# Performance work log

Measured on AMD Instinct MI355X. Metric: run time of the kernel, lower is better.

Reference implementation:

```python
import jax, jax.numpy as jnp
import numpy as np

B, S, E, H, DK, DV, DF = 4, 2048, 512, 8, 64, 64, 2048
EPS = 1e-3  # keras LayerNormalization default epsilon


def setup_inputs() -> dict:
    key = jax.random.key(0)
    ks = jax.random.split(key, 24)
    def n(k, shape, scale=0.02):
        return jax.random.normal(k, shape, jnp.float32) * scale
    inp = {}
    inp["x"] = jax.random.normal(ks[0], (B, S, E), jnp.float32)
    inp["encoder_output"] = jax.random.normal(ks[1], (B, S, E), jnp.float32)
    # lookahead mask: 1 above the diagonal (masked), broadcast over batch/heads
    inp["lookahead_mask"] = jnp.triu(jnp.ones((S, S), jnp.int32), k=1)[None, None]
    # padding mask: 0 = keep (no padding in this synthetic batch)
    inp["padding_mask"] = jnp.zeros((B, 1, 1, S), jnp.int32)
    # self-attention params
    inp["sa_Wq"] = n(ks[2], (E, H * DK)); inp["sa_bq"] = jnp.zeros((H * DK,), jnp.float32)
    inp["sa_Wk"] = n(ks[3], (E, H * DK)); inp["sa_bk"] = jnp.zeros((H * DK,), jnp.float32)
    inp["sa_Wv"] = n(ks[4], (E, H * DV)); inp["sa_bv"] = jnp.zeros((H * DV,), jnp.float32)
    inp["sa_Wo"] = n(ks[5], (H * DV, E)); inp["sa_bo"] = jnp.zeros((E,), jnp.float32)
    # cross-attention params
    inp["ca_Wq"] = n(ks[6], (E, H * DK)); inp["ca_bq"] = jnp.zeros((H * DK,), jnp.float32)
    inp["ca_Wk"] = n(ks[7], (E, H * DK)); inp["ca_bk"] = jnp.zeros((H * DK,), jnp.float32)
    inp["ca_Wv"] = n(ks[8], (E, H * DV)); inp["ca_bv"] = jnp.zeros((H * DV,), jnp.float32)
    inp["ca_Wo"] = n(ks[9], (H * DV, E)); inp["ca_bo"] = jnp.zeros((E,), jnp.float32)
    # feed-forward params
    inp["ff_W1"] = n(ks[10], (E, DF)); inp["ff_b1"] = jnp.zeros((DF,), jnp.float32)
    inp["ff_W2"] = n(ks[11], (DF, E)); inp["ff_b2"] = jnp.zeros((E,), jnp.float32)
    # layernorm params (3 add&norm blocks)
    for i in (1, 2, 3):
        inp[f"ln{i}_g"] = jnp.ones((E,), jnp.float32)
        inp[f"ln{i}_b"] = jnp.zeros((E,), jnp.float32)
    return inp


def _mha(q_in, k_in, v_in, mask, Wq, bq, Wk, bk, Wv, bv, Wo, bo):
    Bq, Sq, _ = q_in.shape
    Sk = k_in.shape[1]
    q = (q_in @ Wq + bq).reshape(Bq, Sq, H, DK).transpose(0, 2, 1, 3)  # bhqd
    k = (k_in @ Wk + bk).reshape(Bq, Sk, H, DK).transpose(0, 2, 1, 3)  # bhkd
    v = (v_in @ Wv + bv).reshape(Bq, Sk, H, DV).transpose(0, 2, 1, 3)  # bhkd
    scores = jnp.einsum("bhqd,bhkd->bhqk", q, k) / jnp.sqrt(jnp.float32(DK))
    scores = scores - 1e9 * mask.astype(scores.dtype)  # additive mask (1 = masked)
    attn = jax.nn.softmax(scores, axis=-1)
    out = jnp.einsum("bhqk,bhkd->bhqd", attn, v)
    out = out.transpose(0, 2, 1, 3).reshape(Bq, Sq, H * DV)
    return out @ Wo + bo


def _add_norm(x, sub, g, b):
    y = x + sub
    m = jnp.mean(y, axis=-1, keepdims=True)
    v = jnp.var(y, axis=-1, keepdims=True)
    return (y - m) / jnp.sqrt(v + EPS) * g + b


def reference(x, encoder_output, lookahead_mask, padding_mask,
              sa_Wq, sa_bq, sa_Wk, sa_bk, sa_Wv, sa_bv, sa_Wo, sa_bo,
              ca_Wq, ca_bq, ca_Wk, ca_bk, ca_Wv, ca_bv, ca_Wo, ca_bo,
              ff_W1, ff_b1, ff_W2, ff_b2,
              ln1_g, ln1_b, ln2_g, ln2_b, ln3_g, ln3_b):
    # dropout is identity at inference (training=False)
    a1 = _mha(x, x, x, lookahead_mask,
              sa_Wq, sa_bq, sa_Wk, sa_bk, sa_Wv, sa_bv, sa_Wo, sa_bo)
    x1 = _add_norm(x, a1, ln1_g, ln1_b)
    a2 = _mha(x1, encoder_output, encoder_output, padding_mask,
              ca_Wq, ca_bq, ca_Wk, ca_bk, ca_Wv, ca_bv, ca_Wo, ca_bo)
    x2 = _add_norm(x1, a2, ln2_g, ln2_b)
    ff = jax.nn.relu(x2 @ ff_W1 + ff_b1) @ ff_W2 + ff_b2
    return _add_norm(x2, ff, ln3_g, ln3_b)
```

## Files before the change

### kernel.cpp

```cpp
#include <hip/hip_runtime.h>

#define Bx  4
#define Sx  2048
#define Ex  512
#define Hx  8
#define Tt  (Bx * Sx)

typedef short          short8 __attribute__((ext_vector_type(8)));
typedef float          f32x4  __attribute__((ext_vector_type(4)));
typedef unsigned short u16;

__device__ __forceinline__ u16 f2bf(float f) {
    unsigned int u = __float_as_uint(f);
    u += 0x7fffu + ((u >> 16) & 1u);
    return (u16)(u >> 16);
}
__device__ __forceinline__ float bf2f(u16 h) {
    return __uint_as_float(((unsigned int)h) << 16);
}

__global__ __launch_bounds__(256) void f32_to_bf16(const float* __restrict__ in,
                                                   u16* __restrict__ out)
{
    int i = (blockIdx.x * 256 + threadIdx.x) << 2;
    float4 v = *(const float4*)(in + i);
    ushort4 o;
    o.x = f2bf(v.x); o.y = f2bf(v.y); o.z = f2bf(v.z); o.w = f2bf(v.w);
    *(ushort4*)(out + i) = o;
}

__global__ __launch_bounds__(256) void transpose_bf16(const float* __restrict__ W,
                                                      u16* __restrict__ Wt,
                                                      int K, int N)
{
    __shared__ u16 tile[32][33];
    const int n0 = blockIdx.x * 32, k0 = blockIdx.y * 32;
    const int tx = threadIdx.x & 31, ty = threadIdx.x >> 5;
#pragma unroll
    for (int i = 0; i < 32; i += 8)
        tile[ty + i][tx] = f2bf(W[(size_t)(k0 + ty + i) * N + n0 + tx]);
    __syncthreads();
#pragma unroll
    for (int i = 0; i < 32; i += 8)
        Wt[(size_t)(n0 + ty + i) * K + k0 + tx] = tile[tx][ty + i];
}

template<int OUT_BF16, int RELU>
__global__ __launch_bounds__(256) void gemm_mfma(const u16* __restrict__ A,
                                                 const u16* __restrict__ Bt,
                                                 const float* __restrict__ bias,
                                                 void* __restrict__ Cout,
                                                 int M, int N, int K)
{
    __shared__ u16 As[128 * 40];
    __shared__ u16 Bs[128 * 40];

    const int tid  = threadIdx.x;
    const int w    = tid >> 6;
    const int lane = tid & 63;
    const int c    = lane & 15;
    const int quad = lane >> 4;
    const int wr   = w >> 1, wc = w & 1;
    const int m0   = blockIdx.y * 128;
    const int n0   = blockIdx.x * 128;

    const int row0 = tid >> 2;
    const int kc   = (tid & 3) << 3;

    const u16* Ap = A  + (size_t)(m0 + row0) * K + kc;
    const u16* Bp = Bt + (size_t)(n0 + row0) * K + kc;
    const size_t rstep = (size_t)64 * K;

    f32x4 acc[4][4];
#pragma unroll
    for (int i = 0; i < 4; i++)
#pragma unroll
        for (int j = 0; j < 4; j++) { acc[i][j][0]=0.f; acc[i][j][1]=0.f; acc[i][j][2]=0.f; acc[i][j][3]=0.f; }

    short8 ra0 = *(const short8*)(Ap);
    short8 ra1 = *(const short8*)(Ap + rstep);
    short8 rb0 = *(const short8*)(Bp);
    short8 rb1 = *(const short8*)(Bp + rstep);

    for (int k0 = 0; k0 < K; k0 += 32) {
        __syncthreads();
        *(short8*)&As[row0 * 40 + kc]        = ra0;
        *(short8*)&As[(row0 + 64) * 40 + kc] = ra1;
        *(short8*)&Bs[row0 * 40 + kc]        = rb0;
        *(short8*)&Bs[(row0 + 64) * 40 + kc] = rb1;
        __syncthreads();

        if (k0 + 32 < K) {
            ra0 = *(const short8*)(Ap + k0 + 32);
            ra1 = *(const short8*)(Ap + rstep + k0 + 32);
            rb0 = *(const short8*)(Bp + k0 + 32);
            rb1 = *(const short8*)(Bp + rstep + k0 + 32);
        }

        short8 af[4], bf[4];
#pragma unroll
        for (int i = 0; i < 4; i++)
            af[i] = *(const short8*)&As[(wr * 64 + i * 16 + c) * 40 + quad * 8];
#pragma unroll
        for (int j = 0; j < 4; j++)
            bf[j] = *(const short8*)&Bs[(wc * 64 + j * 16 + c) * 40 + quad * 8];
#pragma unroll
        for (int i = 0; i < 4; i++)
#pragma unroll
            for (int j = 0; j < 4; j++)
                acc[i][j] = __builtin_amdgcn_mfma_f32_16x16x32_bf16(af[i], bf[j], acc[i][j], 0, 0, 0);
    }

    float bv[4];
#pragma unroll
    for (int j = 0; j < 4; j++) bv[j] = bias[n0 + wc * 64 + j * 16 + c];

#pragma unroll
    for (int i = 0; i < 4; i++) {
#pragma unroll
        for (int j = 0; j < 4; j++) {
            int colg = n0 + wc * 64 + j * 16 + c;
#pragma unroll
            for (int r = 0; r < 4; r++) {
                int rowg = m0 + wr * 64 + i * 16 + quad * 4 + r;
                float v = acc[i][j][r] + bv[j];
                if (RELU) v = fmaxf(v, 0.f);
                if (OUT_BF16) ((u16*)Cout)[(size_t)rowg * N + colg] = f2bf(v);
                else          ((float*)Cout)[(size_t)rowg * N + colg] = v;
            }
        }
    }
}

template<bool CAUSAL>
__global__ __launch_bounds__(256) void attn_mfma(const u16* __restrict__ Q,
                                                 const u16* __restrict__ K,
                                                 const u16* __restrict__ V,
                                                 u16* __restrict__ O)
{
    __shared__ u16 Klds[32 * 72];
    __shared__ u16 Vtlds[64 * 40];
    __shared__ u16 Plds[4][16 * 40];

    const int tid  = threadIdx.x;
    const int w    = tid >> 6;
    const int lane = tid & 63;
    const int c    = lane & 15;
    const int quad = lane >> 4;
    const int q0   = blockIdx.x * 64;
    const int bh   = blockIdx.y;
    const int b    = bh >> 3;
    const int h    = bh & 7;
    const int bS   = b * Sx;
    const int hoff = h * 64;

    const int kkey = tid >> 3;
    const int kc8  = (tid & 7) << 3;
    const int vdim = tid & 63;
    const int vkg  = tid >> 6;

    const u16* qp = Q + (size_t)(bS + q0 + w * 16 + c) * Ex + hoff;
    short8 qa[2];
    qa[0] = *(const short8*)(qp + quad * 8);
    qa[1] = *(const short8*)(qp + 32 + quad * 8);

    f32x4 of[4];
#pragma unroll
    for (int f = 0; f < 4; f++) { of[f][0]=0.f; of[f][1]=0.f; of[f][2]=0.f; of[f][3]=0.f; }
    float lpart[4] = {0.f, 0.f, 0.f, 0.f};

    const int kend = CAUSAL ? (q0 + 64) : Sx;
    for (int kt = 0; kt < kend; kt += 32) {
        __syncthreads();
        *(short8*)&Klds[kkey * 72 + kc8] =
            *(const short8*)(K + (size_t)(bS + kt + kkey) * Ex + hoff + kc8);
        {
            const u16* gv = V + (size_t)(bS + kt + vkg * 8) * Ex + hoff + vdim;
            union { short8 v; u16 u[8]; } vb;
#pragma unroll
            for (int j = 0; j < 8; j++) vb.u[j] = gv[(size_t)j * Ex];
            *(short8*)&Vtlds[vdim * 40 + vkg * 8] = vb.v;
        }
        __syncthreads();

        f32x4 s[2];
#pragma unroll
        for (int kf = 0; kf < 2; kf++) {
            short8 kb0 = *(const short8*)&Klds[(kf * 16 + c) * 72 + quad * 8];
            short8 kb1 = *(const short8*)&Klds[(kf * 16 + c) * 72 + 32 + quad * 8];
            f32x4 z; z[0]=0.f; z[1]=0.f; z[2]=0.f; z[3]=0.f;
            z = __builtin_amdgcn_mfma_f32_16x16x32_bf16(qa[0], kb0, z, 0, 0, 0);
            z = __builtin_amdgcn_mfma_f32_16x16x32_bf16(qa[1], kb1, z, 0, 0, 0);
            s[kf] = z;
        }

#pragma unroll
        for (int kf = 0; kf < 2; kf++) {
            int key_abs = kt + kf * 16 + c;
#pragma unroll
            for (int r = 0; r < 4; r++) {
                float p;
                if (CAUSAL && key_abs > (q0 + w * 16 + quad * 4 + r)) p = 0.f;
                else p = __expf(s[kf][r] * 0.125f);
                u16 pb = f2bf(p);
                lpart[r] += bf2f(pb);
                Plds[w][(quad * 4 + r) * 40 + kf * 16 + c] = pb;
            }
        }
        __threadfence_block();

        short8 pa = *(const short8*)&Plds[w][c * 40 + quad * 8];
#pragma unroll
        for (int f = 0; f < 4; f++) {
            int dim = f * 16 + c;
            short8 vb = *(const short8*)&Vtlds[dim * 40 + quad * 8];
            of[f] = __builtin_amdgcn_mfma_f32_16x16x32_bf16(pa, vb, of[f], 0, 0, 0);
        }
    }

#pragma unroll
    for (int r = 0; r < 4; r++) {
        float v = lpart[r];
        v += __shfl_xor(v, 1, 64);
        v += __shfl_xor(v, 2, 64);
        v += __shfl_xor(v, 4, 64);
        v += __shfl_xor(v, 8, 64);
        lpart[r] = 1.f / v;
    }

    u16* Ob = O + (size_t)(bS + q0 + w * 16) * Ex + hoff;
#pragma unroll
    for (int f = 0; f < 4; f++) {
#pragma unroll
        for (int r = 0; r < 4; r++) {
            Ob[(size_t)(quad * 4 + r) * Ex + f * 16 + c] = f2bf(of[f][r] * lpart[r]);
        }
    }
}

__global__ __launch_bounds__(256) void ln_add(const float* __restrict__ x,
                                              const float* __restrict__ s,
                                              const float* __restrict__ g,
                                              const float* __restrict__ bta,
                                              float* __restrict__ out,
                                              u16* __restrict__ out_bf)
{
    __shared__ float red[8];
    const int    row  = blockIdx.x;
    const int    t    = threadIdx.x;
    const size_t base = (size_t)row * Ex;

    float2 xv = *(const float2*)(x + base + (t << 1));
    float2 sv = *(const float2*)(s + base + (t << 1));
    float  y0 = xv.x + sv.x;
    float  y1 = xv.y + sv.y;

    float sum = y0 + y1;
    float sq  = y0 * y0 + y1 * y1;
#pragma unroll
    for (int o = 32; o > 0; o >>= 1) {
        sum += __shfl_down(sum, o, 64);
        sq  += __shfl_down(sq,  o, 64);
    }
    const int wid = t >> 6, lane = t & 63;
    if (lane == 0) { red[wid] = sum; red[4 + wid] = sq; }
    __syncthreads();
    if (t == 0) {
        red[0] = red[0] + red[1] + red[2] + red[3];
        red[4] = red[4] + red[5] + red[6] + red[7];
    }
    __syncthreads();

    const float mean = red[0] * (1.f / 512.f);
    const float var  = red[4] * (1.f / 512.f) - mean * mean;
    const float rstd = rsqrtf(var + 1e-3f);

    float2 gv = *(const float2*)(g   + (t << 1));
    float2 bv = *(const float2*)(bta + (t << 1));
    float  o0 = (y0 - mean) * rstd * gv.x + bv.x;
    float  o1 = (y1 - mean) * rstd * gv.y + bv.y;
    *(float2*)(out + base + (t << 1)) = make_float2(o0, o1);
    if (out_bf) {
        ushort2 ob; ob.x = f2bf(o0); ob.y = f2bf(o1);
        *(ushort2*)(out_bf + base + (t << 1)) = ob;
    }
}

extern "C" void kernel_launch(void* const* d_in, const int* in_sizes, int n_in,
                              void* d_out, int out_size, void* d_ws, size_t ws_size,
                              hipStream_t stream)
{
    const float* x     = (const float*)d_in[0];
    const float* enc   = (const float*)d_in[1];
    const float* sa_Wq = (const float*)d_in[4],  *sa_bq = (const float*)d_in[5];
    const float* sa_Wk = (const float*)d_in[6],  *sa_bk = (const float*)d_in[7];
    const float* sa_Wv = (const float*)d_in[8],  *sa_bv = (const float*)d_in[9];
    const float* sa_Wo = (const float*)d_in[10], *sa_bo = (const float*)d_in[11];
    const float* ca_Wq = (const float*)d_in[12], *ca_bq = (const float*)d_in[13];
    const float* ca_Wk = (const float*)d_in[14], *ca_bk = (const float*)d_in[15];
    const float* ca_Wv = (const float*)d_in[16], *ca_bv = (const float*)d_in[17];
    const float* ca_Wo = (const float*)d_in[18], *ca_bo = (const float*)d_in[19];
    const float* ff_W1 = (const float*)d_in[20], *ff_b1 = (const float*)d_in[21];
    const float* ff_W2 = (const float*)d_in[22], *ff_b2 = (const float*)d_in[23];
    const float* ln1_g = (const float*)d_in[24], *ln1_b = (const float*)d_in[25];
    const float* ln2_g = (const float*)d_in[26], *ln2_b = (const float*)d_in[27];
    const float* ln3_g = (const float*)d_in[28], *ln3_b = (const float*)d_in[29];

    char* ws = (char*)d_ws;
    const size_t MB = 1024 * 1024;
    u16*   bw   = (u16*)(ws);
    u16*   xb   = (u16*)(ws + 8  * MB);
    u16*   encb = (u16*)(ws + 16 * MB);
    u16*   qb   = (u16*)(ws + 24 * MB);
    u16*   kb   = (u16*)(ws + 32 * MB);
    u16*   vb   = (u16*)(ws + 40 * MB);
    u16*   ob   = (u16*)(ws + 48 * MB);
    float* proj = (float*)(ws + 56 * MB);
    float* x1f  = (float*)(ws + 72 * MB);
    u16*   x1b  = (u16*)(ws + 88 * MB);
    float* x2f  = (float*)(ws + 8  * MB);
    u16*   x2b  = (u16*)(ws + 48 * MB);
    u16*   ff1b = (u16*)(ws + 56 * MB);
    float* ff2f = (float*)(ws + 24 * MB);

    u16* wsaq = bw;                 u16* wsak = bw + 262144;
    u16* wsav = bw + 524288;        u16* wsao = bw + 786432;
    u16* wcaq = bw + 1048576;       u16* wcak = bw + 1310720;
    u16* wcav = bw + 1572864;       u16* wcao = bw + 1835008;
    u16* wff1 = bw + 2097152;       u16* wff2 = bw + 3145728;

    f32_to_bf16<<<dim3(Tt * Ex / 1024), dim3(256), 0, stream>>>(x,   xb);
    f32_to_bf16<<<dim3(Tt * Ex / 1024), dim3(256), 0, stream>>>(enc, encb);
    auto TR = [&](const float* W, u16* Wt, int K, int N) {
        transpose_bf16<<<dim3(N / 32, K / 32), dim3(256), 0, stream>>>(W, Wt, K, N);
    };
    TR(sa_Wq, wsaq, 512, 512);  TR(sa_Wk, wsak, 512, 512);
    TR(sa_Wv, wsav, 512, 512);  TR(sa_Wo, wsao, 512, 512);
    TR(ca_Wq, wcaq, 512, 512);  TR(ca_Wk, wcak, 512, 512);
    TR(ca_Wv, wcav, 512, 512);  TR(ca_Wo, wcao, 512, 512);
    TR(ff_W1, wff1, 512, 2048); TR(ff_W2, wff2, 2048, 512);

    auto GEMM_BF = [&](const u16* A, const u16* Wt, const float* bi, u16* C,
                       int M, int N, int K, bool relu) {
        dim3 grid(N / 128, M / 128);
        if (relu) gemm_mfma<1, 1><<<grid, dim3(256), 0, stream>>>(A, Wt, bi, C, M, N, K);
        else      gemm_mfma<1, 0><<<grid, dim3(256), 0, stream>>>(A, Wt, bi, C, M, N, K);
    };
    auto GEMM_F32 = [&](const u16* A, const u16* Wt, const float* bi, float* C,
                        int M, int N, int K) {
        dim3 grid(N / 128, M / 128);
        gemm_mfma<0, 0><<<grid, dim3(256), 0, stream>>>(A, Wt, bi, C, M, N, K);
    };
    const dim3 agrid(Sx / 64, Bx * Hx);

    GEMM_BF(xb, wsaq, sa_bq, qb, Tt, 512, 512, false);
    GEMM_BF(xb, wsak, sa_bk, kb, Tt, 512, 512, false);
    GEMM_BF(xb, wsav, sa_bv, vb, Tt, 512, 512, false);
    attn_mfma<true><<<agrid, dim3(256), 0, stream>>>(qb, kb, vb, ob);
    GEMM_F32(ob, wsao, sa_bo, proj, Tt, 512, 512);
    ln_add<<<dim3(Tt), dim3(256), 0, stream>>>(x, proj, ln1_g, ln1_b, x1f, x1b);

    GEMM_BF(x1b,  wcaq, ca_bq, qb, Tt, 512, 512, false);
    GEMM_BF(encb, wcak, ca_bk, kb, Tt, 512, 512, false);
    GEMM_BF(encb, wcav, ca_bv, vb, Tt, 512, 512, false);
    attn_mfma<false><<<agrid, dim3(256), 0, stream>>>(qb, kb, vb, ob);
    GEMM_F32(ob, wcao, ca_bo, proj, Tt, 512, 512);
    ln_add<<<dim3(Tt), dim3(256), 0, stream>>>(x1f, proj, ln2_g, ln2_b, x2f, x2b);

    GEMM_BF(x2b, wff1, ff_b1, ff1b, Tt, 2048, 512, true);
    GEMM_F32(ff1b, wff2, ff_b2, ff2f, Tt, 512, 2048);
    ln_add<<<dim3(Tt), dim3(256), 0, stream>>>(x2f, ff2f, ln3_g, ln3_b,
                                               (float*)d_out, (u16*)nullptr);
}
```

Measured before the change: 538.1 us.

## Retile GEMM to 128x64 two-wave blocks and widen attention to 128 queries

The GEMM now uses 128-thread blocks computing 128x64 tiles (each wave 64x64) and takes a leading-dimension argument. Q/K/V projections write into interleaved buffers so attention reads strided rows. The attention kernel now gives each wave 32 query rows, sharing K/V LDS tiles across twice the queries, packs P as bf16 pairs, and skips fully masked causal subtiles. The aim is less K/V reload traffic and better MFMA reuse. The costs are an extra block-wide barrier per key tile, fewer waves per GEMM block, and half as many attention blocks.

```diff
diff --git a/kernel.cpp b/kernel.cpp
--- a/kernel.cpp
+++ b/kernel.cpp
@@ -8,6 +8,7 @@
 
 typedef short          short8 __attribute__((ext_vector_type(8)));
 typedef float          f32x4  __attribute__((ext_vector_type(4)));
+typedef unsigned int   u32x4  __attribute__((ext_vector_type(4)));
 typedef unsigned short u16;
 
 __device__ __forceinline__ u16 f2bf(float f) {
@@ -46,30 +47,29 @@
 }
 
 template<int OUT_BF16, int RELU>
-__global__ __launch_bounds__(256) void gemm_mfma(const u16* __restrict__ A,
+__global__ __launch_bounds__(128) void gemm_mfma(const u16* __restrict__ A,
                                                  const u16* __restrict__ Bt,
                                                  const float* __restrict__ bias,
                                                  void* __restrict__ Cout,
-                                                 int M, int N, int K)
+                                                 int M, int N, int K, int ldc)
 {
     __shared__ u16 As[128 * 40];
-    __shared__ u16 Bs[128 * 40];
+    __shared__ u16 Bs[64 * 40];
 
     const int tid  = threadIdx.x;
     const int w    = tid >> 6;
     const int lane = tid & 63;
     const int c    = lane & 15;
     const int quad = lane >> 4;
-    const int wr   = w >> 1, wc = w & 1;
     const int m0   = blockIdx.y * 128;
-    const int n0   = blockIdx.x * 128;
-
-    const int row0 = tid >> 2;
-    const int kc   = (tid & 3) << 3;
-
-    const u16* Ap = A  + (size_t)(m0 + row0) * K + kc;
-    const u16* Bp = Bt + (size_t)(n0 + row0) * K + kc;
-    const size_t rstep = (size_t)64 * K;
+    const int n0   = blockIdx.x * 64;
+
+    const int rA = tid >> 2;
+    const int kc = (tid & 3) << 3;
+
+    const u16* Ap = A  + (size_t)(m0 + rA) * K + kc;
+    const u16* Bp = Bt + (size_t)(n0 + rA) * K + kc;
+    const size_t a32 = (size_t)32 * K;
 
     f32x4 acc[4][4];
 #pragma unroll
@@ -77,33 +77,34 @@
 #pragma unroll
         for (int j = 0; j < 4; j++) { acc[i][j][0]=0.f; acc[i][j][1]=0.f; acc[i][j][2]=0.f; acc[i][j][3]=0.f; }
 
-    short8 ra0 = *(const short8*)(Ap);
-    short8 ra1 = *(const short8*)(Ap + rstep);
-    short8 rb0 = *(const short8*)(Bp);
-    short8 rb1 = *(const short8*)(Bp + rstep);
+    short8 ra[4], rb[2];
+#pragma unroll
+    for (int i = 0; i < 4; i++) ra[i] = *(const short8*)(Ap + i * a32);
+#pragma unroll
+    for (int i = 0; i < 2; i++) rb[i] = *(const short8*)(Bp + i * a32);
 
     for (int k0 = 0; k0 < K; k0 += 32) {
         __syncthreads();
-        *(short8*)&As[row0 * 40 + kc]        = ra0;
-        *(short8*)&As[(row0 + 64) * 40 + kc] = ra1;
-        *(short8*)&Bs[row0 * 40 + kc]        = rb0;
-        *(short8*)&Bs[(row0 + 64) * 40 + kc] = rb1;
+#pragma unroll
+        for (int i = 0; i < 4; i++) *(short8*)&As[(rA + i * 32) * 40 + kc] = ra[i];
+#pragma unroll
+        for (int i = 0; i < 2; i++) *(short8*)&Bs[(rA + i * 32) * 40 + kc] = rb[i];
         __syncthreads();
 
         if (k0 + 32 < K) {
-            ra0 = *(const short8*)(Ap + k0 + 32);
-            ra1 = *(const short8*)(Ap + rstep + k0 + 32);
-            rb0 = *(const short8*)(Bp + k0 + 32);
-            rb1 = *(const short8*)(Bp + rstep + k0 + 32);
+#pragma unroll
+            for (int i = 0; i < 4; i++) ra[i] = *(const short8*)(Ap + i * a32 + k0 + 32);
+#pragma unroll
+            for (int i = 0; i < 2; i++) rb[i] = *(const short8*)(Bp + i * a32 + k0 + 32);
         }
 
         short8 af[4], bf[4];
 #pragma unroll
         for (int i = 0; i < 4; i++)
-            af[i] = *(const short8*)&As[(wr * 64 + i * 16 + c) * 40 + quad * 8];
+            af[i] = *(const short8*)&As[(w * 64 + i * 16 + c) * 40 + quad * 8];
 #pragma unroll
         for (int j = 0; j < 4; j++)
-            bf[j] = *(const short8*)&Bs[(wc * 64 + j * 16 + c) * 40 + quad * 8];
+            bf[j] = *(const short8*)&Bs[(j * 16 + c) * 40 + quad * 8];
 #pragma unroll
         for (int i = 0; i < 4; i++)
 #pragma unroll
@@ -113,20 +114,20 @@
 
     float bv[4];
 #pragma unroll
-    for (int j = 0; j < 4; j++) bv[j] = bias[n0 + wc * 64 + j * 16 + c];
+    for (int j = 0; j < 4; j++) bv[j] = bias[n0 + j * 16 + c];
 
 #pragma unroll
     for (int i = 0; i < 4; i++) {
 #pragma unroll
         for (int j = 0; j < 4; j++) {
-            int colg = n0 + wc * 64 + j * 16 + c;
+            int colg = n0 + j * 16 + c;
 #pragma unroll
             for (int r = 0; r < 4; r++) {
-                int rowg = m0 + wr * 64 + i * 16 + quad * 4 + r;
+                int rowg = m0 + w * 64 + i * 16 + quad * 4 + r;
                 float v = acc[i][j][r] + bv[j];
                 if (RELU) v = fmaxf(v, 0.f);
-                if (OUT_BF16) ((u16*)Cout)[(size_t)rowg * N + colg] = f2bf(v);
-                else          ((float*)Cout)[(size_t)rowg * N + colg] = v;
+                if (OUT_BF16) ((u16*)Cout)[(size_t)rowg * ldc + colg] = f2bf(v);
+                else          ((float*)Cout)[(size_t)rowg * ldc + colg] = v;
             }
         }
     }
@@ -136,105 +137,141 @@
 __global__ __launch_bounds__(256) void attn_mfma(const u16* __restrict__ Q,
                                                  const u16* __restrict__ K,
                                                  const u16* __restrict__ V,
-                                                 u16* __restrict__ O)
-{
-    __shared__ u16 Klds[32 * 72];
-    __shared__ u16 Vtlds[64 * 40];
-    __shared__ u16 Plds[4][16 * 40];
+                                                 u16* __restrict__ O,
+                                                 int ldq, int ldk, int ldv)
+{
+    __shared__ u16          Klds[32 * 72];
+    __shared__ u16          Vtlds[64 * 40];
+    __shared__ unsigned int Plds[4][32 * 20];
 
     const int tid  = threadIdx.x;
     const int w    = tid >> 6;
     const int lane = tid & 63;
     const int c    = lane & 15;
     const int quad = lane >> 4;
-    const int q0   = blockIdx.x * 64;
+    const int q0   = blockIdx.x * 128;
     const int bh   = blockIdx.y;
     const int b    = bh >> 3;
     const int h    = bh & 7;
     const int bS   = b * Sx;
     const int hoff = h * 64;
+    const int qw   = q0 + w * 32;
 
     const int kkey = tid >> 3;
     const int kc8  = (tid & 7) << 3;
     const int vdim = tid & 63;
-    const int vkg  = tid >> 6;
-
-    const u16* qp = Q + (size_t)(bS + q0 + w * 16 + c) * Ex + hoff;
-    short8 qa[2];
-    qa[0] = *(const short8*)(qp + quad * 8);
-    qa[1] = *(const short8*)(qp + 32 + quad * 8);
-
-    f32x4 of[4];
-#pragma unroll
-    for (int f = 0; f < 4; f++) { of[f][0]=0.f; of[f][1]=0.f; of[f][2]=0.f; of[f][3]=0.f; }
-    float lpart[4] = {0.f, 0.f, 0.f, 0.f};
-
-    const int kend = CAUSAL ? (q0 + 64) : Sx;
+    const int vp   = (tid >> 6) << 3;
+    const int kb2  = vp >> 1;
+
+    short8 qa[2][2];
+#pragma unroll
+    for (int rf = 0; rf < 2; rf++) {
+        const u16* qp = Q + (size_t)(bS + qw + rf * 16 + c) * ldq + hoff;
+        qa[rf][0] = *(const short8*)(qp + quad * 8);
+        qa[rf][1] = *(const short8*)(qp + 32 + quad * 8);
+    }
+
+    f32x4 of[2][4];
+#pragma unroll
+    for (int rf = 0; rf < 2; rf++)
+#pragma unroll
+        for (int f = 0; f < 4; f++) { of[rf][f][0]=0.f; of[rf][f][1]=0.f; of[rf][f][2]=0.f; of[rf][f][3]=0.f; }
+    float lpart[2][4] = {{0.f,0.f,0.f,0.f},{0.f,0.f,0.f,0.f}};
+
+    const int kend = CAUSAL ? (q0 + 128) : Sx;
     for (int kt = 0; kt < kend; kt += 32) {
         __syncthreads();
         *(short8*)&Klds[kkey * 72 + kc8] =
-            *(const short8*)(K + (size_t)(bS + kt + kkey) * Ex + hoff + kc8);
+            *(const short8*)(K + (size_t)(bS + kt + kkey) * ldk + hoff + kc8);
         {
-            const u16* gv = V + (size_t)(bS + kt + vkg * 8) * Ex + hoff + vdim;
+            const u16* gv = V + (size_t)(bS + kt) * ldv + hoff + vdim;
             union { short8 v; u16 u[8]; } vb;
 #pragma unroll
-            for (int j = 0; j < 8; j++) vb.u[j] = gv[(size_t)j * Ex];
-            *(short8*)&Vtlds[vdim * 40 + vkg * 8] = vb.v;
+            for (int j = 0; j < 8; j++) {
+                int key = kb2 + (j >> 1) + ((j & 1) << 4);
+                vb.u[j] = gv[(size_t)key * ldv];
+            }
+            *(short8*)&Vtlds[vdim * 40 + vp] = vb.v;
         }
         __syncthreads();
 
-        f32x4 s[2];
-#pragma unroll
-        for (int kf = 0; kf < 2; kf++) {
-            short8 kb0 = *(const short8*)&Klds[(kf * 16 + c) * 72 + quad * 8];
-            short8 kb1 = *(const short8*)&Klds[(kf * 16 + c) * 72 + 32 + quad * 8];
-            f32x4 z; z[0]=0.f; z[1]=0.f; z[2]=0.f; z[3]=0.f;
-            z = __builtin_amdgcn_mfma_f32_16x16x32_bf16(qa[0], kb0, z, 0, 0, 0);
-            z = __builtin_amdgcn_mfma_f32_16x16x32_bf16(qa[1], kb1, z, 0, 0, 0);
-            s[kf] = z;
-        }
-
-#pragma unroll
-        for (int kf = 0; kf < 2; kf++) {
-            int key_abs = kt + kf * 16 + c;
-#pragma unroll
-            for (int r = 0; r < 4; r++) {
-                float p;
-                if (CAUSAL && key_abs > (q0 + w * 16 + quad * 4 + r)) p = 0.f;
-                else p = __expf(s[kf][r] * 0.125f);
-                u16 pb = f2bf(p);
-                lpart[r] += bf2f(pb);
-                Plds[w][(quad * 4 + r) * 40 + kf * 16 + c] = pb;
+        const bool live1 = !CAUSAL || (kt <= qw + 31);
+        const bool live0 = !CAUSAL || (kt <= qw + 15);
+
+        if (live1) {
+            short8 kb[2][2];
+#pragma unroll
+            for (int kf = 0; kf < 2; kf++) {
+                kb[kf][0] = *(const short8*)&Klds[(kf * 16 + c) * 72 + quad * 8];
+                kb[kf][1] = *(const short8*)&Klds[(kf * 16 + c) * 72 + 32 + quad * 8];
             }
-        }
-        __threadfence_block();
-
-        short8 pa = *(const short8*)&Plds[w][c * 40 + quad * 8];
-#pragma unroll
-        for (int f = 0; f < 4; f++) {
-            int dim = f * 16 + c;
-            short8 vb = *(const short8*)&Vtlds[dim * 40 + quad * 8];
-            of[f] = __builtin_amdgcn_mfma_f32_16x16x32_bf16(pa, vb, of[f], 0, 0, 0);
-        }
-    }
-
-#pragma unroll
-    for (int r = 0; r < 4; r++) {
-        float v = lpart[r];
-        v += __shfl_xor(v, 1, 64);
-        v += __shfl_xor(v, 2, 64);
-        v += __shfl_xor(v, 4, 64);
-        v += __shfl_xor(v, 8, 64);
-        lpart[r] = 1.f / v;
-    }
-
-    u16* Ob = O + (size_t)(bS + q0 + w * 16) * Ex + hoff;
-#pragma unroll
-    for (int f = 0; f < 4; f++) {
+
+#pragma unroll
+            for (int rf = 0; rf < 2; rf++) {
+                if (rf == 0 && !live0) continue;
+                f32x4 s[2];
+#pragma unroll
+                for (int kf = 0; kf < 2; kf++) {
+                    f32x4 z; z[0]=0.f; z[1]=0.f; z[2]=0.f; z[3]=0.f;
+                    z = __builtin_amdgcn_mfma_f32_16x16x32_bf16(qa[rf][0], kb[kf][0], z, 0, 0, 0);
+                    z = __builtin_amdgcn_mfma_f32_16x16x32_bf16(qa[rf][1], kb[kf][1], z, 0, 0, 0);
+                    s[kf] = z;
+                }
+#pragma unroll
+                for (int r = 0; r < 4; r++) {
+                    int qg = qw + rf * 16 + quad * 4 + r;
+                    float p0, p1;
+                    if (CAUSAL && (kt + c) > qg) p0 = 0.f;
+                    else p0 = __expf(s[0][r] * 0.125f);
+                    if (CAUSAL && (kt + 16 + c) > qg) p1 = 0.f;
+                    else p1 = __expf(s[1][r] * 0.125f);
+                    u16 b0 = f2bf(p0), b1 = f2bf(p1);
+                    lpart[rf][r] += bf2f(b0) + bf2f(b1);
+                    Plds[w][(rf * 16 + quad * 4 + r) * 20 + c] =
+                        (unsigned int)b0 | ((unsigned int)b1 << 16);
+                }
+            }
+        }
+        __syncthreads();
+
+        if (live1) {
+            short8 vb[4];
+#pragma unroll
+            for (int f = 0; f < 4; f++)
+                vb[f] = *(const short8*)&Vtlds[(f * 16 + c) * 40 + quad * 8];
+#pragma unroll
+            for (int rf = 0; rf < 2; rf++) {
+                if (rf == 0 && !live0) continue;
+                union { u32x4 u; short8 s; } pu;
+                pu.u = *(const u32x4*)&Plds[w][(rf * 16 + c) * 20 + quad * 4];
+                short8 pa = pu.s;
+#pragma unroll
+                for (int f = 0; f < 4; f++)
+                    of[rf][f] = __builtin_amdgcn_mfma_f32_16x16x32_bf16(pa, vb[f], of[rf][f], 0, 0, 0);
+            }
+        }
+    }
+
+#pragma unroll
+    for (int rf = 0; rf < 2; rf++)
 #pragma unroll
         for (int r = 0; r < 4; r++) {
-            Ob[(size_t)(quad * 4 + r) * Ex + f * 16 + c] = f2bf(of[f][r] * lpart[r]);
-        }
+            float v = lpart[rf][r];
+            v += __shfl_xor(v, 1, 64);
+            v += __shfl_xor(v, 2, 64);
+            v += __shfl_xor(v, 4, 64);
+            v += __shfl_xor(v, 8, 64);
+            lpart[rf][r] = 1.f / v;
+        }
+
+#pragma unroll
+    for (int rf = 0; rf < 2; rf++) {
+        u16* Ob = O + (size_t)(bS + qw + rf * 16) * Ex + hoff;
+#pragma unroll
+        for (int f = 0; f < 4; f++)
+#pragma unroll
+            for (int r = 0; r < 4; r++)
+                Ob[(size_t)(quad * 4 + r) * Ex + f * 16 + c] = f2bf(of[rf][f][r] * lpart[rf][r]);
     }
 }
 
@@ -311,17 +348,16 @@
     u16*   bw   = (u16*)(ws);
     u16*   xb   = (u16*)(ws + 8  * MB);
     u16*   encb = (u16*)(ws + 16 * MB);
+    u16*   qkvB = (u16*)(ws + 24 * MB);
     u16*   qb   = (u16*)(ws + 24 * MB);
-    u16*   kb   = (u16*)(ws + 32 * MB);
-    u16*   vb   = (u16*)(ws + 40 * MB);
+    u16*   kvB  = (u16*)(ws + 32 * MB);
+    u16*   ff1b = (u16*)(ws + 24 * MB);
     u16*   ob   = (u16*)(ws + 48 * MB);
-    float* proj = (float*)(ws + 56 * MB);
+    float* projF= (float*)(ws + 56 * MB);
     float* x1f  = (float*)(ws + 72 * MB);
     u16*   x1b  = (u16*)(ws + 88 * MB);
+    u16*   x2b  = (u16*)(ws + 88 * MB);
     float* x2f  = (float*)(ws + 8  * MB);
-    u16*   x2b  = (u16*)(ws + 48 * MB);
-    u16*   ff1b = (u16*)(ws + 56 * MB);
-    float* ff2f = (float*)(ws + 24 * MB);
 
     u16* wsaq = bw;                 u16* wsak = bw + 262144;
     u16* wsav = bw + 524288;        u16* wsao = bw + 786432;
@@ -340,35 +376,34 @@
     TR(ca_Wv, wcav, 512, 512);  TR(ca_Wo, wcao, 512, 512);
     TR(ff_W1, wff1, 512, 2048); TR(ff_W2, wff2, 2048, 512);
 
-    auto GEMM_BF = [&](const u16* A, const u16* Wt, const float* bi, u16* C,
-                       int M, int N, int K, bool relu) {
-        dim3 grid(N / 128, M / 128);
-        if (relu) gemm_mfma<1, 1><<<grid, dim3(256), 0, stream>>>(A, Wt, bi, C, M, N, K);
-        else      gemm_mfma<1, 0><<<grid, dim3(256), 0, stream>>>(A, Wt, bi, C, M, N, K);
+    auto GEMM = [&](const u16* A, const u16* Wt, const float* bi, void* C,
+                    int N, int K, int ldc, int out_bf, int relu) {
+        dim3 grid(N / 64, Tt / 128);
+        if (out_bf) {
+            if (relu) gemm_mfma<1,1><<<grid, dim3(128), 0, stream>>>(A, Wt, bi, C, Tt, N, K, ldc);
+            else      gemm_mfma<1,0><<<grid, dim3(128), 0, stream>>>(A, Wt, bi, C, Tt, N, K, ldc);
+        } else        gemm_mfma<0,0><<<grid, dim3(128), 0, stream>>>(A, Wt, bi, C, Tt, N, K, ldc);
     };
-    auto GEMM_F32 = [&](const u16* A, const u16* Wt, const float* bi, float* C,
-                        int M, int N, int K) {
-        dim3 grid(N / 128, M / 128);
-        gemm_mfma<0, 0><<<grid, dim3(256), 0, stream>>>(A, Wt, bi, C, M, N, K);
-    };
-    const dim3 agrid(Sx / 64, Bx * Hx);
-
-    GEMM_BF(xb, wsaq, sa_bq, qb, Tt, 512, 512, false);
-    GEMM_BF(xb, wsak, sa_bk, kb, Tt, 512, 512, false);
-    GEMM_BF(xb, wsav, sa_bv, vb, Tt, 512, 512, false);
-    attn_mfma<true><<<agrid, dim3(256), 0, stream>>>(qb, kb, vb, ob);
-    GEMM_F32(ob, wsao, sa_bo, proj, Tt, 512, 512);
-    ln_add<<<dim3(Tt), dim3(256), 0, stream>>>(x, proj, ln1_g, ln1_b, x1f, x1b);
-
-    GEMM_BF(x1b,  wcaq, ca_bq, qb, Tt, 512, 512, false);
-    GEMM_BF(encb, wcak, ca_bk, kb, Tt, 512, 512, false);
-    GEMM_BF(encb, wcav, ca_bv, vb, Tt, 512, 512, false);
-    attn_mfma<false><<<agrid, dim3(256), 0, stream>>>(qb, kb, vb, ob);
-    GEMM_F32(ob, wcao, ca_bo, proj, Tt, 512, 512);
-    ln_add<<<dim3(Tt), dim3(256), 0, stream>>>(x1f, proj, ln2_g, ln2_b, x2f, x2b);
-
-    GEMM_BF(x2b, wff1, ff_b1, ff1b, Tt, 2048, 512, true);
-    GEMM_F32(ff1b, wff2, ff_b2, ff2f, Tt, 512, 2048);
-    ln_add<<<dim3(Tt), dim3(256), 0, stream>>>(x2f, ff2f, ln3_g, ln3_b,
+    const dim3 agrid(Sx / 128, Bx * Hx);
+
+    GEMM(xb, wsaq, sa_bq, qkvB,        512, 512, 1536, 1, 0);
+    GEMM(xb, wsak, sa_bk, qkvB + 512,  512, 512, 1536, 1, 0);
+    GEMM(xb, wsav, sa_bv, qkvB + 1024, 512, 512, 1536, 1, 0);
+    attn_mfma<true><<<agrid, dim3(256), 0, stream>>>(qkvB, qkvB + 512, qkvB + 1024,
+                                                     ob, 1536, 1536, 1536);
+    GEMM(ob, wsao, sa_bo, projF, 512, 512, 512, 0, 0);
+    ln_add<<<dim3(Tt), dim3(256), 0, stream>>>(x, projF, ln1_g, ln1_b, x1f, x1b);
+
+    GEMM(x1b,  wcaq, ca_bq, qb,        512, 512, 512,  1, 0);
+    GEMM(encb, wcak, ca_bk, kvB,       512, 512, 1024, 1, 0);
+    GEMM(encb, wcav, ca_bv, kvB + 512, 512, 512, 1024, 1, 0);
+    attn_mfma<false><<<agrid, dim3(256), 0, stream>>>(qb, kvB, kvB + 512,
+                                                      ob, 512, 1024, 1024);
+    GEMM(ob, wcao, ca_bo, projF, 512, 512, 512, 0, 0);
+    ln_add<<<dim3(Tt), dim3(256), 0, stream>>>(x1f, projF, ln2_g, ln2_b, x2f, x2b);
+
+    GEMM(x2b, wff1, ff_b1, ff1b, 2048, 512, 2048, 1, 1);
+    GEMM(ff1b, wff2, ff_b2, projF, 512, 2048, 512, 0, 0);
+    ln_add<<<dim3(Tt), dim3(256), 0, stream>>>(x2f, projF, ln3_g, ln3_b,
                                                (float*)d_out, (u16*)nullptr);
 }
```

Result: slower. 583.1 us (+8.4%).

## Widen attention key tiles to 64, skip masked causal blocks, batch prep launches

Applied to the files above, without the earlier changes.

The attention kernel now processes 64 keys per iteration instead of 32, with larger K and V LDS tiles and a permuted V-transpose layout, so each P fragment packs two score blocks into 32-bit LDS words. It skips QK and PV MFMAs for 16-key blocks that lie entirely above the causal diagonal. Q/K/V projections write into interleaved strided buffers, and the input conversion and eight weight transposes are merged into fewer launches. The intent is to cut loop and synchronisation overhead per key and avoid wasted work on masked blocks. In exchange, LDS use per block is higher and the wave-local fence is replaced by a full __syncthreads.

```diff
diff --git a/kernel.cpp b/kernel.cpp
--- a/kernel.cpp
+++ b/kernel.cpp
@@ -8,6 +8,7 @@
 
 typedef short          short8 __attribute__((ext_vector_type(8)));
 typedef float          f32x4  __attribute__((ext_vector_type(4)));
+typedef unsigned int   u32x4  __attribute__((ext_vector_type(4)));
 typedef unsigned short u16;
 
 __device__ __forceinline__ u16 f2bf(float f) {
@@ -19,9 +20,13 @@
     return __uint_as_float(((unsigned int)h) << 16);
 }
 
-__global__ __launch_bounds__(256) void f32_to_bf16(const float* __restrict__ in,
-                                                   u16* __restrict__ out)
-{
+__global__ __launch_bounds__(256) void f32_to_bf16_2(const float* __restrict__ a,
+                                                     const float* __restrict__ b,
+                                                     u16* __restrict__ oa,
+                                                     u16* __restrict__ ob)
+{
+    const float* in  = blockIdx.y ? b : a;
+    u16*         out = blockIdx.y ? ob : oa;
     int i = (blockIdx.x * 256 + threadIdx.x) << 2;
     float4 v = *(const float4*)(in + i);
     ushort4 o;
@@ -45,12 +50,29 @@
         Wt[(size_t)(n0 + ty + i) * K + k0 + tx] = tile[tx][ty + i];
 }
 
+struct WPtrs { const float* w[8]; };
+__global__ __launch_bounds__(256) void transpose8_bf16(WPtrs ws, u16* __restrict__ base)
+{
+    __shared__ u16 tile[32][33];
+    const float* W  = ws.w[blockIdx.z];
+    u16*         Wt = base + (size_t)blockIdx.z * 262144;
+    const int n0 = blockIdx.x * 32, k0 = blockIdx.y * 32;
+    const int tx = threadIdx.x & 31, ty = threadIdx.x >> 5;
+#pragma unroll
+    for (int i = 0; i < 32; i += 8)
+        tile[ty + i][tx] = f2bf(W[(size_t)(k0 + ty + i) * 512 + n0 + tx]);
+    __syncthreads();
+#pragma unroll
+    for (int i = 0; i < 32; i += 8)
+        Wt[(size_t)(n0 + ty + i) * 512 + k0 + tx] = tile[tx][ty + i];
+}
+
 template<int OUT_BF16, int RELU>
 __global__ __launch_bounds__(256) void gemm_mfma(const u16* __restrict__ A,
                                                  const u16* __restrict__ Bt,
                                                  const float* __restrict__ bias,
                                                  void* __restrict__ Cout,
-                                                 int M, int N, int K)
+                                                 int M, int N, int K, int ldc)
 {
     __shared__ u16 As[128 * 40];
     __shared__ u16 Bs[128 * 40];
@@ -125,8 +147,8 @@
                 int rowg = m0 + wr * 64 + i * 16 + quad * 4 + r;
                 float v = acc[i][j][r] + bv[j];
                 if (RELU) v = fmaxf(v, 0.f);
-                if (OUT_BF16) ((u16*)Cout)[(size_t)rowg * N + colg] = f2bf(v);
-                else          ((float*)Cout)[(size_t)rowg * N + colg] = v;
+                if (OUT_BF16) ((u16*)Cout)[(size_t)rowg * ldc + colg] = f2bf(v);
+                else          ((float*)Cout)[(size_t)rowg * ldc + colg] = v;
             }
         }
     }
@@ -136,11 +158,12 @@
 __global__ __launch_bounds__(256) void attn_mfma(const u16* __restrict__ Q,
                                                  const u16* __restrict__ K,
                                                  const u16* __restrict__ V,
-                                                 u16* __restrict__ O)
-{
-    __shared__ u16 Klds[32 * 72];
-    __shared__ u16 Vtlds[64 * 40];
-    __shared__ u16 Plds[4][16 * 40];
+                                                 u16* __restrict__ O,
+                                                 int ldq, int ldk, int ldv)
+{
+    __shared__ u16          Klds[64 * 72];
+    __shared__ u16          Vtlds[64 * 72];
+    __shared__ unsigned int Plds[4][16 * 36];
 
     const int tid  = threadIdx.x;
     const int w    = tid >> 6;
@@ -153,16 +176,17 @@
     const int h    = bh & 7;
     const int bS   = b * Sx;
     const int hoff = h * 64;
-
-    const int kkey = tid >> 3;
-    const int kc8  = (tid & 7) << 3;
+    const int qw   = q0 + w * 16;
+
     const int vdim = tid & 63;
-    const int vkg  = tid >> 6;
-
-    const u16* qp = Q + (size_t)(bS + q0 + w * 16 + c) * Ex + hoff;
+    const int vp   = (tid >> 6) << 4;
+
     short8 qa[2];
-    qa[0] = *(const short8*)(qp + quad * 8);
-    qa[1] = *(const short8*)(qp + 32 + quad * 8);
+    {
+        const u16* qp = Q + (size_t)(bS + qw + c) * ldq + hoff;
+        qa[0] = *(const short8*)(qp + quad * 8);
+        qa[1] = *(const short8*)(qp + 32 + quad * 8);
+    }
 
     f32x4 of[4];
 #pragma unroll
@@ -170,51 +194,88 @@
     float lpart[4] = {0.f, 0.f, 0.f, 0.f};
 
     const int kend = CAUSAL ? (q0 + 64) : Sx;
-    for (int kt = 0; kt < kend; kt += 32) {
+    for (int kt = 0; kt < kend; kt += 64) {
         __syncthreads();
-        *(short8*)&Klds[kkey * 72 + kc8] =
-            *(const short8*)(K + (size_t)(bS + kt + kkey) * Ex + hoff + kc8);
+#pragma unroll
+        for (int i = 0; i < 2; i++) {
+            int chunk = tid + (i << 8);
+            int row   = chunk >> 3;
+            int c8    = (chunk & 7) << 3;
+            *(short8*)&Klds[row * 72 + c8] =
+                *(const short8*)(K + (size_t)(bS + kt + row) * ldk + hoff + c8);
+        }
         {
-            const u16* gv = V + (size_t)(bS + kt + vkg * 8) * Ex + hoff + vdim;
-            union { short8 v; u16 u[8]; } vb;
-#pragma unroll
-            for (int j = 0; j < 8; j++) vb.u[j] = gv[(size_t)j * Ex];
-            *(short8*)&Vtlds[vdim * 40 + vkg * 8] = vb.v;
+            const u16* gv = V + (size_t)(bS + kt) * ldv + hoff + vdim;
+            union { short8 v; u16 u[8]; } v0, v1;
+#pragma unroll
+            for (int j = 0; j < 8; j++) {
+                int pos = vp + j;
+                int g = pos >> 5, pp = pos & 31;
+                v0.u[j] = gv[(size_t)((g << 5) + (pp >> 1) + ((pp & 1) << 4)) * ldv];
+            }
+#pragma unroll
+            for (int j = 0; j < 8; j++) {
+                int pos = vp + 8 + j;
+                int g = pos >> 5, pp = pos & 31;
+                v1.u[j] = gv[(size_t)((g << 5) + (pp >> 1) + ((pp & 1) << 4)) * ldv];
+            }
+            *(short8*)&Vtlds[vdim * 72 + vp]     = v0.v;
+            *(short8*)&Vtlds[vdim * 72 + vp + 8] = v1.v;
         }
         __syncthreads();
 
-        f32x4 s[2];
-#pragma unroll
-        for (int kf = 0; kf < 2; kf++) {
-            short8 kb0 = *(const short8*)&Klds[(kf * 16 + c) * 72 + quad * 8];
-            short8 kb1 = *(const short8*)&Klds[(kf * 16 + c) * 72 + 32 + quad * 8];
-            f32x4 z; z[0]=0.f; z[1]=0.f; z[2]=0.f; z[3]=0.f;
-            z = __builtin_amdgcn_mfma_f32_16x16x32_bf16(qa[0], kb0, z, 0, 0, 0);
-            z = __builtin_amdgcn_mfma_f32_16x16x32_bf16(qa[1], kb1, z, 0, 0, 0);
-            s[kf] = z;
-        }
-
-#pragma unroll
-        for (int kf = 0; kf < 2; kf++) {
-            int key_abs = kt + kf * 16 + c;
-#pragma unroll
-            for (int r = 0; r < 4; r++) {
-                float p;
-                if (CAUSAL && key_abs > (q0 + w * 16 + quad * 4 + r)) p = 0.f;
-                else p = __expf(s[kf][r] * 0.125f);
-                u16 pb = f2bf(p);
-                lpart[r] += bf2f(pb);
-                Plds[w][(quad * 4 + r) * 40 + kf * 16 + c] = pb;
-            }
-        }
-        __threadfence_block();
-
-        short8 pa = *(const short8*)&Plds[w][c * 40 + quad * 8];
+        int fmax = 4;
+        if (CAUSAL) {
+            int d = ((qw + 15 - kt) >> 4) + 1;
+            fmax = d < 4 ? d : 4;
+        }
+
+        f32x4 s[4];
 #pragma unroll
         for (int f = 0; f < 4; f++) {
-            int dim = f * 16 + c;
-            short8 vb = *(const short8*)&Vtlds[dim * 40 + quad * 8];
-            of[f] = __builtin_amdgcn_mfma_f32_16x16x32_bf16(pa, vb, of[f], 0, 0, 0);
+            if (f < fmax) {
+                short8 kb0 = *(const short8*)&Klds[(f * 16 + c) * 72 + quad * 8];
+                short8 kb1 = *(const short8*)&Klds[(f * 16 + c) * 72 + 32 + quad * 8];
+                f32x4 z; z[0]=0.f; z[1]=0.f; z[2]=0.f; z[3]=0.f;
+                z = __builtin_amdgcn_mfma_f32_16x16x32_bf16(qa[0], kb0, z, 0, 0, 0);
+                z = __builtin_amdgcn_mfma_f32_16x16x32_bf16(qa[1], kb1, z, 0, 0, 0);
+                s[f] = z;
+            }
+        }
+
+#pragma unroll
+        for (int fp = 0; fp < 2; fp++) {
+            if (fp * 2 < fmax) {
+                int f0 = fp * 2, f1 = fp * 2 + 1;
+#pragma unroll
+                for (int r = 0; r < 4; r++) {
+                    int qg = qw + quad * 4 + r;
+                    float p0 = 0.f, p1 = 0.f;
+                    if (!(CAUSAL && (kt + f0 * 16 + c) > qg))
+                        p0 = __expf(s[f0][r] * 0.125f);
+                    if (f1 < fmax && !(CAUSAL && (kt + f1 * 16 + c) > qg))
+                        p1 = __expf(s[f1][r] * 0.125f);
+                    u16 b0 = f2bf(p0), b1 = f2bf(p1);
+                    lpart[r] += bf2f(b0) + bf2f(b1);
+                    Plds[w][(quad * 4 + r) * 36 + fp * 18 + c] =
+                        (unsigned int)b0 | ((unsigned int)b1 << 16);
+                }
+            }
+        }
+        __syncthreads();
+
+#pragma unroll
+        for (int g = 0; g < 2; g++) {
+            if (g * 2 < fmax) {
+                union { u32x4 u; short8 s; } pu;
+                pu.u = *(const u32x4*)&Plds[w][c * 36 + g * 18 + quad * 4];
+                short8 pa = pu.s;
+#pragma unroll
+                for (int f2 = 0; f2 < 4; f2++) {
+                    short8 vbf = *(const short8*)&Vtlds[(f2 * 16 + c) * 72 + (g << 5) + quad * 8];
+                    of[f2] = __builtin_amdgcn_mfma_f32_16x16x32_bf16(pa, vbf, of[f2], 0, 0, 0);
+                }
+            }
         }
     }
 
@@ -228,14 +289,12 @@
         lpart[r] = 1.f / v;
     }
 
-    u16* Ob = O + (size_t)(bS + q0 + w * 16) * Ex + hoff;
-#pragma unroll
-    for (int f = 0; f < 4; f++) {
-#pragma unroll
-        for (int r = 0; r < 4; r++) {
+    u16* Ob = O + (size_t)(bS + qw) * Ex + hoff;
+#pragma unroll
+    for (int f = 0; f < 4; f++)
+#pragma unroll
+        for (int r = 0; r < 4; r++)
             Ob[(size_t)(quad * 4 + r) * Ex + f * 16 + c] = f2bf(of[f][r] * lpart[r]);
-        }
-    }
 }
 
 __global__ __launch_bounds__(256) void ln_add(const float* __restrict__ x,
@@ -311,17 +370,16 @@
     u16*   bw   = (u16*)(ws);
     u16*   xb   = (u16*)(ws + 8  * MB);
     u16*   encb = (u16*)(ws + 16 * MB);
+    u16*   qkvB = (u16*)(ws + 24 * MB);
     u16*   qb   = (u16*)(ws + 24 * MB);
-    u16*   kb   = (u16*)(ws + 32 * MB);
-    u16*   vb   = (u16*)(ws + 40 * MB);
+    u16*   kvB  = (u16*)(ws + 32 * MB);
+    u16*   ff1b = (u16*)(ws + 24 * MB);
     u16*   ob   = (u16*)(ws + 48 * MB);
-    float* proj = (float*)(ws + 56 * MB);
+    float* projF= (float*)(ws + 56 * MB);
     float* x1f  = (float*)(ws + 72 * MB);
     u16*   x1b  = (u16*)(ws + 88 * MB);
+    u16*   x2b  = (u16*)(ws + 88 * MB);
     float* x2f  = (float*)(ws + 8  * MB);
-    u16*   x2b  = (u16*)(ws + 48 * MB);
-    u16*   ff1b = (u16*)(ws + 56 * MB);
-    float* ff2f = (float*)(ws + 24 * MB);
 
     u16* wsaq = bw;                 u16* wsak = bw + 262144;
     u16* wsav = bw + 524288;        u16* wsao = bw + 786432;
@@ -329,46 +387,41 @@
     u16* wcav = bw + 1572864;       u16* wcao = bw + 1835008;
     u16* wff1 = bw + 2097152;       u16* wff2 = bw + 3145728;
 
-    f32_to_bf16<<<dim3(Tt * Ex / 1024), dim3(256), 0, stream>>>(x,   xb);
-    f32_to_bf16<<<dim3(Tt * Ex / 1024), dim3(256), 0, stream>>>(enc, encb);
-    auto TR = [&](const float* W, u16* Wt, int K, int N) {
-        transpose_bf16<<<dim3(N / 32, K / 32), dim3(256), 0, stream>>>(W, Wt, K, N);
-    };
-    TR(sa_Wq, wsaq, 512, 512);  TR(sa_Wk, wsak, 512, 512);
-    TR(sa_Wv, wsav, 512, 512);  TR(sa_Wo, wsao, 512, 512);
-    TR(ca_Wq, wcaq, 512, 512);  TR(ca_Wk, wcak, 512, 512);
-    TR(ca_Wv, wcav, 512, 512);  TR(ca_Wo, wcao, 512, 512);
-    TR(ff_W1, wff1, 512, 2048); TR(ff_W2, wff2, 2048, 512);
-
-    auto GEMM_BF = [&](const u16* A, const u16* Wt, const float* bi, u16* C,
-                       int M, int N, int K, bool relu) {
-        dim3 grid(N / 128, M / 128);
-        if (relu) gemm_mfma<1, 1><<<grid, dim3(256), 0, stream>>>(A, Wt, bi, C, M, N, K);
-        else      gemm_mfma<1, 0><<<grid, dim3(256), 0, stream>>>(A, Wt, bi, C, M, N, K);
-    };
-    auto GEMM_F32 = [&](const u16* A, const u16* Wt, const float* bi, float* C,
-                        int M, int N, int K) {
-        dim3 grid(N / 128, M / 128);
-        gemm_mfma<0, 0><<<grid, dim3(256), 0, stream>>>(A, Wt, bi, C, M, N, K);
+    f32_to_bf16_2<<<dim3(Tt * Ex / 1024, 2), dim3(256), 0, stream>>>(x, enc, xb, encb);
+    WPtrs wp; wp.w[0]=sa_Wq; wp.w[1]=sa_Wk; wp.w[2]=sa_Wv; wp.w[3]=sa_Wo;
+    wp.w[4]=ca_Wq; wp.w[5]=ca_Wk; wp.w[6]=ca_Wv; wp.w[7]=ca_Wo;
+    transpose8_bf16<<<dim3(16, 16, 8), dim3(256), 0, stream>>>(wp, bw);
+    transpose_bf16<<<dim3(64, 16), dim3(256), 0, stream>>>(ff_W1, wff1, 512, 2048);
+    transpose_bf16<<<dim3(16, 64), dim3(256), 0, stream>>>(ff_W2, wff2, 2048, 512);
+
+    auto GEMM = [&](const u16* A, const u16* Wt, const float* bi, void* C,
+                    int N, int K, int ldc, int out_bf, int relu) {
+        dim3 grid(N / 128, Tt / 128);
+        if (out_bf) {
+            if (relu) gemm_mfma<1,1><<<grid, dim3(256), 0, stream>>>(A, Wt, bi, C, Tt, N, K, ldc);
+            else      gemm_mfma<1,0><<<grid, dim3(256), 0, stream>>>(A, Wt, bi, C, Tt, N, K, ldc);
+        } else        gemm_mfma<0,0><<<grid, dim3(256), 0, stream>>>(A, Wt, bi, C, Tt, N, K, ldc);
     };
     const dim3 agrid(Sx / 64, Bx * Hx);
 
-    GEMM_BF(xb, wsaq, sa_bq, qb, Tt, 512, 512, false);
-    GEMM_BF(xb, wsak, sa_bk, kb, Tt, 512, 512, false);
-    GEMM_BF(xb, wsav, sa_bv, vb, Tt, 512, 512, false);
-    attn_mfma<true><<<agrid, dim3(256), 0, stream>>>(qb, kb, vb, ob);
-    GEMM_F32(ob, wsao, sa_bo, proj, Tt, 512, 512);
-    ln_add<<<dim3(Tt), dim3(256), 0, stream>>>(x, proj, ln1_g, ln1_b, x1f, x1b);
-
-    GEMM_BF(x1b,  wcaq, ca_bq, qb, Tt, 512, 512, false);
-    GEMM_BF(encb, wcak, ca_bk, kb, Tt, 512, 512, false);
-    GEMM_BF(encb, wcav, ca_bv, vb, Tt, 512, 512, false);
-    attn_mfma<false><<<agrid, dim3(256), 0, stream>>>(qb, kb, vb, ob);
-    GEMM_F32(ob, wcao, ca_bo, proj, Tt, 512, 512);
-    ln_add<<<dim3(Tt), dim3(256), 0, stream>>>(x1f, proj, ln2_g, ln2_b, x2f, x2b);
-
-    GEMM_BF(x2b, wff1, ff_b1, ff1b, Tt, 2048, 512, true);
-    GEMM_F32(ff1b, wff2, ff_b2, ff2f, Tt, 512, 2048);
-    ln_add<<<dim3(Tt), dim3(256), 0, stream>>>(x2f, ff2f, ln3_g, ln3_b,
+    GEMM(xb, wsaq, sa_bq, qkvB,        512, 512, 1536, 1, 0);
+    GEMM(xb, wsak, sa_bk, qkvB + 512,  512, 512, 1536, 1, 0);
+    GEMM(xb, wsav, sa_bv, qkvB + 1024, 512, 512, 1536, 1, 0);
+    attn_mfma<true><<<agrid, dim3(256), 0, stream>>>(qkvB, qkvB + 512, qkvB + 1024,
+                                                     ob, 1536, 1536, 1536);
+    GEMM(ob, wsao, sa_bo, projF, 512, 512, 512, 0, 0);
+    ln_add<<<dim3(Tt), dim3(256), 0, stream>>>(x, projF, ln1_g, ln1_b, x1f, x1b);
+
+    GEMM(x1b,  wcaq, ca_bq, qb,        512, 512, 512,  1, 0);
+    GEMM(encb, wcak, ca_bk, kvB,       512, 512, 1024, 1, 0);
+    GEMM(encb, wcav, ca_bv, kvB + 512, 512, 512, 1024, 1, 0);
+    attn_mfma<false><<<agrid, dim3(256), 0, stream>>>(qb, kvB, kvB + 512,
+                                                      ob, 512, 1024, 1024);
+    GEMM(ob, wcao, ca_bo, projF, 512, 512, 512, 0, 0);
+    ln_add<<<dim3(Tt), dim3(256), 0, stream>>>(x1f, projF, ln2_g, ln2_b, x2f, x2b);
+
+    GEMM(x2b, wff1, ff_b1, ff1b, 2048, 512, 2048, 1, 1);
+    GEMM(ff1b, wff2, ff_b2, projF, 512, 2048, 512, 0, 0);
+    ln_add<<<dim3(Tt), dim3(256), 0, stream>>>(x2f, projF, ln3_g, ln3_b,
                                                (float*)d_out, (u16*)nullptr);
 }
```

Measured after the change: 553.8 us. 1.03x slower.
